# Optimization experiments

Hardware: AMD Instinct MI355X
Metric: run time of the kernel (lower is better)

Reference implementation:

```python
import jax, jax.numpy as jnp
import numpy as np

EPS_ROW = 1e-8
EPS_BN = 1e-5


def _row_norm(A):
    # A / clamp(rowsum, 1e-8)
    return A / jnp.clip(A.sum(axis=1, keepdims=True), EPS_ROW, None)


def _bn_eval(x, gamma, beta, mean, var):
    return (x - mean) * (gamma / jnp.sqrt(var + EPS_BN)) + beta


def setup_inputs() -> dict:
    key = jax.random.key(0)
    ks = jax.random.split(key, 12)
    n_src, n_tgt = 8192, 16384
    d_src, d_tgt_in, d_hid, d_out = 256, 128, 128, 64

    def xavier(k, fan_in, fan_out):
        lim = float(np.sqrt(6.0 / (fan_in + fan_out)))
        # stored as [in, out] so forward is x @ W + b
        return jax.random.uniform(k, (fan_in, fan_out), jnp.float32, -lim, lim)

    inp = {
        "H_source": jax.random.normal(ks[0], (n_src, d_src), jnp.float32),
        "H_target": jax.random.normal(ks[1], (n_tgt, d_tgt_in), jnp.float32),
        "A": jax.random.uniform(ks[2], (n_tgt, n_src), jnp.float32),
        "W0": xavier(ks[3], d_src, d_hid),
        "b0": jnp.zeros((d_hid,), jnp.float32),
        "Wb0": xavier(ks[4], d_hid, d_hid),
        "bb0": jnp.zeros((d_hid,), jnp.float32),
        "W1": xavier(ks[5], d_hid, d_hid),
        "b1": jnp.zeros((d_hid,), jnp.float32),
        # fwd BN layers (i=0 and i=2): stacked [2, d_hid]
        "bn_f_gamma": jax.random.uniform(ks[6], (2, d_hid), jnp.float32, 0.5, 1.5),
        "bn_f_beta": jax.random.normal(ks[7], (2, d_hid), jnp.float32) * 0.1,
        "bn_f_mean": jax.random.normal(ks[8], (2, d_hid), jnp.float32) * 0.1,
        "bn_f_var": jax.random.uniform(ks[9], (2, d_hid), jnp.float32, 0.5, 1.5),
        # bwd BN layer (i=1)
        "bn_b_gamma": jax.random.uniform(ks[10], (d_hid,), jnp.float32, 0.5, 1.5),
        "bn_b_beta": jnp.zeros((d_hid,), jnp.float32),
        "bn_b_mean": jnp.zeros((d_hid,), jnp.float32),
        "bn_b_var": jnp.ones((d_hid,), jnp.float32),
        "Wout": xavier(ks[11], d_hid, d_out),
        "bout": jnp.zeros((d_out,), jnp.float32),
    }
    return inp


def reference(H_source, H_target, A, W0, b0, Wb0, bb0, W1, b1,
              bn_f_gamma, bn_f_beta, bn_f_mean, bn_f_var,
              bn_b_gamma, bn_b_beta, bn_b_mean, bn_b_var,
              Wout, bout):
    # Inference mode: dropout = identity, BatchNorm uses running stats.
    A_n = _row_norm(A)          # [n_tgt, n_src]
    AT_n = _row_norm(A.T)       # [n_src, n_tgt]

    # layer 0 (fwd): target <- source
    h_tgt = (A_n @ H_source) @ W0 + b0
    h_tgt = jax.nn.relu(_bn_eval(h_tgt, bn_f_gamma[0], bn_f_beta[0], bn_f_mean[0], bn_f_var[0]))

    # layer 1 (bwd): source <- target
    h_src = (AT_n @ h_tgt) @ Wb0 + bb0
    h_src = jax.nn.relu(_bn_eval(h_src, bn_b_gamma, bn_b_beta, bn_b_mean, bn_b_var))

    # layer 2 (fwd): target <- source
    h_tgt = (A_n @ h_src) @ W1 + b1
    h_tgt = jax.nn.relu(_bn_eval(h_tgt, bn_f_gamma[1], bn_f_beta[1], bn_f_mean[1], bn_f_var[1]))

    return h_tgt @ Wout + bout  # [n_tgt, d_out]
```

## Files before the change

### kernel.cpp

```cpp
#include <hip/hip_runtime.h>
#include <hip/hip_bf16.h>
#include <stdint.h>

typedef unsigned short ushort_t;
typedef float   f32x4  __attribute__((ext_vector_type(4)));
typedef short   bf16x8 __attribute__((ext_vector_type(8)));

#define NSRC 8192
#define NTGT 16384

__device__ __forceinline__ ushort_t f2bf(float f){
  union { float f; uint32_t u; } v; v.f = f;
  uint32_t r = v.u + 0x7fffu + ((v.u >> 16) & 1u);
  return (ushort_t)(r >> 16);
}
__device__ __forceinline__ uint2 pack4(f32x4 v){
  uint2 r;
  r.x = (uint32_t)f2bf(v.x) | ((uint32_t)f2bf(v.y) << 16);
  r.y = (uint32_t)f2bf(v.z) | ((uint32_t)f2bf(v.w) << 16);
  return r;
}
__device__ __forceinline__ bf16x8 cvt8(f32x4 lo, f32x4 hi){
  union { uint4 u; bf16x8 h; } x;
  uint2 a = pack4(lo), b = pack4(hi);
  x.u = make_uint4(a.x, a.y, b.x, b.y);
  return x.h;
}
__device__ __forceinline__ uint4 asu4(bf16x8 v){ union { bf16x8 h; uint4 u; } x; x.h = v; return x.u; }
__device__ __forceinline__ float sum4(f32x4 v){ return v.x + v.y + v.z + v.w; }

typedef __attribute__((address_space(1))) const uint32_t* gas_t;
typedef __attribute__((address_space(3))) uint32_t* las_t;
__device__ __forceinline__ void dma16(const void* g, void* l){
  __builtin_amdgcn_global_load_lds((gas_t)g, (las_t)l, 16, 0, 0);
}
#define SCHED_FENCE() __builtin_amdgcn_sched_barrier(0)

__global__ __launch_bounds__(256) void k_wt(const float* __restrict__ S, ushort_t* __restrict__ D,
                                            int R, int C){
  __shared__ float tile[32][33];
  const int cb = blockIdx.x * 32, rb = blockIdx.y * 32;
  const int tx = threadIdx.x & 31, ty = threadIdx.x >> 5;
#pragma unroll
  for (int i = 0; i < 4; ++i)
    tile[ty + 8*i][tx] = S[(size_t)(rb + ty + 8*i) * C + cb + tx];
  __syncthreads();
#pragma unroll
  for (int i = 0; i < 4; ++i)
    D[(size_t)(cb + ty + 8*i) * R + rb + tx] = f2bf(tile[tx][ty + 8*i]);
}

__global__ __launch_bounds__(256) void k_packH(const float* __restrict__ S, ushort_t* __restrict__ D){
  int u = blockIdx.x * 4 + (threadIdx.x >> 6);
  int lane = threadIdx.x & 63;
  int nb = u >> 8, kb = u & 255;
  int fr = lane & 15, q = lane >> 4;
  ushort_t buf[8];
#pragma unroll
  for (int j = 0; j < 8; ++j)
    buf[j] = f2bf(S[(size_t)(kb * 32 + q * 8 + j) * 256 + nb * 16 + fr]);
  *(uint4*)&D[((size_t)nb * 256 + kb) * 512 + (size_t)lane * 8] = *(uint4*)buf;
}

__global__ void k_init_b2p_tail(ushort_t* __restrict__ B2p){
  int idx = blockIdx.x * 256 + threadIdx.x;
  int lane = idx & 63;
  int kb = idx >> 6;
  int fr = lane & 15;
  uint32_t v = (fr == 0) ? 0x3F803F80u : 0u;
  uint4 val = {v, v, v, v};
  *(uint4*)&B2p[((size_t)8 * 512 + kb) * 512 + (size_t)lane * 8] = val;
}

__global__ __launch_bounds__(512) void k_gemm1(const float* __restrict__ A,
    const ushort_t* __restrict__ B1p, float* __restrict__ P2, float* __restrict__ rowsumP,
    ushort_t* __restrict__ Abf){
  __shared__ ushort_t Bls[2][16 * 512];
  const int t = threadIdx.x;
  const int mb = blockIdx.x, kc = blockIdx.y;
  const size_t m0 = (size_t)mb * 128;
  const int k0 = kc * 2048;
  const int kb0 = k0 >> 5;

  const int w = t >> 6, lane = t & 63;
  const int wr = w >> 1, wc = w & 1;
  const int fr = lane & 15, q = lane >> 4;

  const float* pa0 = &A[(m0 + wr * 32 + fr) * (size_t)NSRC + k0 + q * 8];
  const float* pa1 = pa0 + (size_t)16 * NSRC;
  ushort_t* pw0 = &Abf[(m0 + wr * 32 + fr) * (size_t)NSRC + k0 + q * 8];
  ushort_t* pw1 = pw0 + (size_t)16 * NSRC;
  ushort_t* pw  = (wc == 0) ? pw0 : pw1;

  f32x4 acc[2][8];
  const f32x4 vz = {0.f, 0.f, 0.f, 0.f};
#pragma unroll
  for (int i = 0; i < 2; ++i)
#pragma unroll
    for (int j = 0; j < 8; ++j) acc[i][j] = vz;
  float rs0 = 0.f, rs1 = 0.f;

#pragma unroll
  for (int i = 0; i < 2; ++i){
    int f = w * 2 + i;
    dma16(&B1p[((size_t)f * 256 + kb0) * 512 + (size_t)lane * 8], &Bls[0][f * 512]);
  }
  SCHED_FENCE();
  f32x4 c0a = *(const f32x4*)pa0,        c0b = *(const f32x4*)(pa0 + 4);
  f32x4 c1a = *(const f32x4*)pa1,        c1b = *(const f32x4*)(pa1 + 4);
  f32x4 d0a = *(const f32x4*)(pa0 + 32), d0b = *(const f32x4*)(pa0 + 36);
  f32x4 d1a = *(const f32x4*)(pa1 + 32), d1b = *(const f32x4*)(pa1 + 36);
  asm volatile("s_waitcnt vmcnt(8)" ::: "memory");
  SCHED_FENCE();
  __builtin_amdgcn_s_barrier();

  for (int kt = 0; kt < 64; ++kt){
    const int cur = kt & 1;
    rs0 += sum4(c0a) + sum4(c0b);
    rs1 += sum4(c1a) + sum4(c1b);
    bf16x8 af0 = cvt8(c0a, c0b);
    bf16x8 af1 = cvt8(c1a, c1b);

    if (kt < 63){
#pragma unroll
      for (int i = 0; i < 2; ++i){
        int f = w * 2 + i;
        dma16(&B1p[((size_t)f * 256 + kb0 + kt + 1) * 512 + (size_t)lane * 8],
              &Bls[cur ^ 1][f * 512]);
      }
    }
    SCHED_FENCE();
    c0a = d0a; c0b = d0b; c1a = d1a; c1b = d1b;
    if (kt < 62){
      d0a = *(const f32x4*)(pa0 + (kt + 2) * 32); d0b = *(const f32x4*)(pa0 + (kt + 2) * 32 + 4);
      d1a = *(const f32x4*)(pa1 + (kt + 2) * 32); d1b = *(const f32x4*)(pa1 + (kt + 2) * 32 + 4);
    }
    *(uint4*)&pw[kt * 32] = asu4(wc == 0 ? af0 : af1);

#pragma unroll
    for (int fn = 0; fn < 8; ++fn){
      bf16x8 bfv = *(bf16x8*)&Bls[cur][(wc * 8 + fn) * 512 + lane * 8];
      acc[0][fn] = __builtin_amdgcn_mfma_f32_16x16x32_bf16(af0, bfv, acc[0][fn], 0, 0, 0);
      acc[1][fn] = __builtin_amdgcn_mfma_f32_16x16x32_bf16(af1, bfv, acc[1][fn], 0, 0, 0);
    }
    asm volatile("s_waitcnt vmcnt(5)" ::: "memory");
    SCHED_FENCE();
    __builtin_amdgcn_s_barrier();
  }

  float* Pd = P2 + (size_t)kc * NTGT * 256;
#pragma unroll
  for (int fm = 0; fm < 2; ++fm)
#pragma unroll
    for (int j = 0; j < 4; ++j){
      int row = wr * 32 + fm * 16 + q * 4 + j;
#pragma unroll
      for (int fn = 0; fn < 8; ++fn)
        Pd[(m0 + row) * 256 + wc * 128 + fn * 16 + fr] = acc[fm][fn][j];
    }

  rs0 += __shfl_xor(rs0, 16); rs0 += __shfl_xor(rs0, 32);
  rs1 += __shfl_xor(rs1, 16); rs1 += __shfl_xor(rs1, 32);
  if (wc == 0 && q == 0){
    rowsumP[(size_t)kc * NTGT + m0 + wr * 32 + fr]      = rs0;
    rowsumP[(size_t)kc * NTGT + m0 + wr * 32 + 16 + fr] = rs1;
  }
}

__global__ __launch_bounds__(512) void k_gemm2(const ushort_t* __restrict__ Abf,
    const ushort_t* __restrict__ B2p, float* __restrict__ G2p){
  __shared__ ushort_t Bls[2][9 * 512];
  const int t = threadIdx.x;
  const int sb = blockIdx.x, kc = blockIdx.y;
  const size_t s0 = (size_t)sb * 128;
  const int k0 = kc * 2048;
  const int kb0 = k0 >> 5;

  const int w = t >> 6, lane = t & 63;
  const int fr = lane & 15, q = lane >> 4;
  const size_t scol = s0 + w * 16 + fr;
  const ushort_t* pA = &Abf[(size_t)(k0 + q * 8) * NSRC + scol];

  f32x4 acc[9];
  const f32x4 vz = {0.f, 0.f, 0.f, 0.f};
#pragma unroll
  for (int j = 0; j < 9; ++j) acc[j] = vz;

#pragma unroll
  for (int i = 0; i < 2; ++i){
    int f = w + i * 8;
    if (f < 9)
      dma16(&B2p[((size_t)f * 512 + kb0) * 512 + (size_t)lane * 8], &Bls[0][f * 512]);
  }
  SCHED_FENCE();
  ushort_t aN[8], aX[8];
#pragma unroll
  for (int j = 0; j < 8; ++j) aN[j] = pA[(size_t)j * NSRC];
#pragma unroll
  for (int j = 0; j < 8; ++j) aX[j] = pA[(size_t)(32 + j) * NSRC];
  asm volatile("s_waitcnt vmcnt(16)" ::: "memory");
  SCHED_FENCE();
  __builtin_amdgcn_s_barrier();

  for (int kt = 0; kt < 64; ++kt){
    const int cur = kt & 1;
    bf16x8 af;
#pragma unroll
    for (int j = 0; j < 8; ++j) af[j] = (short)aN[j];

    if (kt < 63){
#pragma unroll
      for (int i = 0; i < 2; ++i){
        int f = w + i * 8;
        if (f < 9)
          dma16(&B2p[((size_t)f * 512 + kb0 + kt + 1) * 512 + (size_t)lane * 8],
                &Bls[cur ^ 1][f * 512]);
      }
    }
    SCHED_FENCE();
#pragma unroll
    for (int j = 0; j < 8; ++j) aN[j] = aX[j];
    if (kt < 62){
#pragma unroll
      for (int j = 0; j < 8; ++j)
        aX[j] = pA[((size_t)(kt + 2) * 32 + j) * NSRC];
    }

#pragma unroll
    for (int fn = 0; fn < 9; ++fn){
      bf16x8 bfv = *(bf16x8*)&Bls[cur][fn * 512 + lane * 8];
      acc[fn] = __builtin_amdgcn_mfma_f32_16x16x32_bf16(af, bfv, acc[fn], 0, 0, 0);
    }
    asm volatile("s_waitcnt vmcnt(8)" ::: "memory");
    SCHED_FENCE();
    __builtin_amdgcn_s_barrier();
  }

  float* Pd = G2p + (size_t)kc * NSRC * 144;
#pragma unroll
  for (int j = 0; j < 4; ++j){
    int row = w * 16 + q * 4 + j;
#pragma unroll
    for (int fn = 0; fn < 9; ++fn)
      Pd[(s0 + row) * 144 + fn * 16 + fr] = acc[fn][j];
  }
}

__global__ __launch_bounds__(512) void k_gemm3(const ushort_t* __restrict__ Abf,
    const ushort_t* __restrict__ B3p, float* __restrict__ G3p){
  __shared__ ushort_t Bls[2][8 * 512];
  const int t = threadIdx.x;
  const int mb = blockIdx.x, kc = blockIdx.y;
  const size_t m0 = (size_t)mb * 128;
  const int k0 = kc * 2048;
  const int kb0 = k0 >> 5;

  const int w = t >> 6, lane = t & 63;
  const int wr = w >> 1, wc = w & 1;
  const int fr = lane & 15, q = lane >> 4;

  const ushort_t* pa0 = &Abf[(m0 + wr * 32 + fr) * (size_t)NSRC + k0 + q * 8];
  const ushort_t* pa1 = pa0 + (size_t)16 * NSRC;

  f32x4 acc[2][4];
  const f32x4 vz = {0.f, 0.f, 0.f, 0.f};
#pragma unroll
  for (int i = 0; i < 2; ++i)
#pragma unroll
    for (int j = 0; j < 4; ++j) acc[i][j] = vz;

  dma16(&B3p[((size_t)w * 256 + kb0) * 512 + (size_t)lane * 8], &Bls[0][w * 512]);
  SCHED_FENCE();
  bf16x8 a0N = *(const bf16x8*)pa0;
  bf16x8 a1N = *(const bf16x8*)pa1;
  bf16x8 a0X = *(const bf16x8*)(pa0 + 32);
  bf16x8 a1X = *(const bf16x8*)(pa1 + 32);
  asm volatile("s_waitcnt vmcnt(4)" ::: "memory");
  SCHED_FENCE();
  __builtin_amdgcn_s_barrier();

  for (int kt = 0; kt < 64; ++kt){
    const int cur = kt & 1;
    bf16x8 u0 = a0N, u1 = a1N;

    if (kt < 63){
      dma16(&B3p[((size_t)w * 256 + kb0 + kt + 1) * 512 + (size_t)lane * 8],
            &Bls[cur ^ 1][w * 512]);
    }
    SCHED_FENCE();
    a0N = a0X; a1N = a1X;
    if (kt < 62){
      a0X = *(const bf16x8*)(pa0 + (kt + 2) * 32);
      a1X = *(const bf16x8*)(pa1 + (kt + 2) * 32);
    }

#pragma unroll
    for (int fn = 0; fn < 4; ++fn){
      bf16x8 bfv = *(bf16x8*)&Bls[cur][(wc * 4 + fn) * 512 + lane * 8];
      acc[0][fn] = __builtin_amdgcn_mfma_f32_16x16x32_bf16(u0, bfv, acc[0][fn], 0, 0, 0);
      acc[1][fn] = __builtin_amdgcn_mfma_f32_16x16x32_bf16(u1, bfv, acc[1][fn], 0, 0, 0);
    }
    asm volatile("s_waitcnt vmcnt(2)" ::: "memory");
    SCHED_FENCE();
    __builtin_amdgcn_s_barrier();
  }

  float* Pd = G3p + (size_t)kc * NTGT * 128;
#pragma unroll
  for (int fm = 0; fm < 2; ++fm)
#pragma unroll
    for (int j = 0; j < 4; ++j){
      int row = wr * 32 + fm * 16 + q * 4 + j;
#pragma unroll
      for (int fn = 0; fn < 4; ++fn)
        Pd[(m0 + row) * 128 + wc * 64 + fn * 16 + fr] = acc[fm][fn][j];
    }
}

__global__ __launch_bounds__(256) void k_s1(
    const float* __restrict__ P2, const float* __restrict__ rowsumP,
    const ushort_t* __restrict__ W0t, const float* __restrict__ b0,
    const float* __restrict__ g, const float* __restrict__ be,
    const float* __restrict__ mu, const float* __restrict__ va,
    ushort_t* __restrict__ B2p)
{
  __shared__ ushort_t Xs[64 * 72];
  __shared__ ushort_t Ws[128 * 72];
  __shared__ float    os[64 * 132];
  __shared__ float invs[64], scs[128], mbs[128];
  const int t = threadIdx.x;
  const size_t m0 = (size_t)blockIdx.x * 64;
  const size_t CH = (size_t)NTGT * 256;

  if (t < 64){
    float rsv = rowsumP[m0 + t] + rowsumP[(size_t)NTGT + m0 + t]
              + rowsumP[2 * (size_t)NTGT + m0 + t] + rowsumP[3 * (size_t)NTGT + m0 + t];
    invs[t] = 1.0f / fmaxf(rsv, 1e-8f);
  } else if (t < 192){
    int n = t - 64;
    float s = g[n] * rsqrtf(va[n] + 1e-5f);
    scs[n] = s;
    mbs[n] = (b0[n] - mu[n]) * s + be[n];
  }
  __syncthreads();

  const int w = t >> 6, lane = t & 63;
  const int wr = w >> 1, wc = w & 1;
  const int fr = lane & 15, q = lane >> 4;
  f32x4 acc[2][4];
  const f32x4 vz = {0.f, 0.f, 0.f, 0.f};
#pragma unroll
  for (int i = 0; i < 2; ++i)
#pragma unroll
    for (int j = 0; j < 4; ++j) acc[i][j] = vz;

  for (int kt = 0; kt < 4; ++kt){
    const int kk = kt * 64;
    __syncthreads();
#pragma unroll
    for (int r = 0; r < 4; ++r){
      int c = t + 256 * r;
      int row = c >> 4, col4 = (c & 15) * 4;
      const float* pa = &P2[(m0 + row) * 256 + kk + col4];
      f32x4 v0 = *(const f32x4*)pa;
      f32x4 v1 = *(const f32x4*)(pa + CH);
      f32x4 v2 = *(const f32x4*)(pa + 2 * CH);
      f32x4 v3 = *(const f32x4*)(pa + 3 * CH);
      f32x4 v = (v0 + v1 + v2 + v3) * invs[row];
      *(uint2*)&Xs[row * 72 + col4] = pack4(v);
    }
#pragma unroll
    for (int r = 0; r < 4; ++r){
      int c = t + 256 * r;
      int n = c >> 3, k8 = (c & 7) * 8;
      *(uint4*)&Ws[n * 72 + k8] = *(const uint4*)&W0t[(size_t)n * 256 + kk + k8];
    }
    __syncthreads();
#pragma unroll
    for (int ks = 0; ks < 2; ++ks){
      bf16x8 af[2], bfv[4];
      af[0] = *(const bf16x8*)&Xs[(wr * 32 + fr) * 72 + ks * 32 + q * 8];
      af[1] = *(const bf16x8*)&Xs[(wr * 32 + 16 + fr) * 72 + ks * 32 + q * 8];
#pragma unroll
      for (int fn = 0; fn < 4; ++fn)
        bfv[fn] = *(const bf16x8*)&Ws[(wc * 64 + fn * 16 + fr) * 72 + ks * 32 + q * 8];
#pragma unroll
      for (int fm = 0; fm < 2; ++fm)
#pragma unroll
        for (int fn = 0; fn < 4; ++fn)
          acc[fm][fn] = __builtin_amdgcn_mfma_f32_16x16x32_bf16(af[fm], bfv[fn], acc[fm][fn], 0, 0, 0);
    }
  }

#pragma unroll
  for (int fm = 0; fm < 2; ++fm)
#pragma unroll
    for (int fn = 0; fn < 4; ++fn){
      int n = wc * 64 + fn * 16 + fr;
      float s = scs[n], mb = mbs[n];
#pragma unroll
      for (int j = 0; j < 4; ++j){
        int row = wr * 32 + fm * 16 + q * 4 + j;
        os[row * 132 + n] = fmaxf(acc[fm][fn][j] * s + mb, 0.f);
      }
    }
  __syncthreads();
  {
    const int kb0 = (int)(m0 >> 5);
#pragma unroll
    for (int r = 0; r < 4; ++r){
      int s = t + 256 * r;
      int lane2 = s & 63;
      int kb2 = (s >> 6) & 1;
      int nb = s >> 7;
      int fr2 = lane2 & 15, q2 = lane2 >> 4;
      int n = nb * 16 + fr2;
      ushort_t buf[8];
#pragma unroll
      for (int j = 0; j < 8; ++j)
        buf[j] = f2bf(os[(kb2 * 32 + q2 * 8 + j) * 132 + n]);
      *(uint4*)&B2p[((size_t)nb * 512 + kb0 + kb2) * 512 + (size_t)lane2 * 8] = *(uint4*)buf;
    }
  }
}

__global__ __launch_bounds__(256) void k_s2(
    const float* __restrict__ G2p,
    const ushort_t* __restrict__ Wb0t, const float* __restrict__ bb0,
    const float* __restrict__ g, const float* __restrict__ be,
    const float* __restrict__ mu, const float* __restrict__ va,
    ushort_t* __restrict__ B3p)
{
  __shared__ ushort_t Xs[64 * 72];
  __shared__ ushort_t Ws[128 * 72];
  __shared__ float    os[64 * 132];
  __shared__ float invs[64], scs[128], mbs[128];
  const int t = threadIdx.x;
  const size_t m0 = (size_t)blockIdx.x * 64;
  const size_t CH = (size_t)NSRC * 144;

  if (t < 64){
    size_t row = m0 + t;
    float c = 0.f;
#pragma unroll
    for (int i = 0; i < 8; ++i) c += G2p[i * CH + row * 144 + 128];
    invs[t] = 1.0f / fmaxf(c, 1e-8f);
  } else if (t < 192){
    int n = t - 64;
    float s = g[n] * rsqrtf(va[n] + 1e-5f);
    scs[n] = s;
    mbs[n] = (bb0[n] - mu[n]) * s + be[n];
  }
  __syncthreads();

  const int w = t >> 6, lane = t & 63;
  const int wr = w >> 1, wc = w & 1;
  const int fr = lane & 15, q = lane >> 4;
  f32x4 acc[2][4];
  const f32x4 vz = {0.f, 0.f, 0.f, 0.f};
#pragma unroll
  for (int i = 0; i < 2; ++i)
#pragma unroll
    for (int j = 0; j < 4; ++j) acc[i][j] = vz;

  for (int kt = 0; kt < 2; ++kt){
    const int kk = kt * 64;
    __syncthreads();
#pragma unroll
    for (int r = 0; r < 4; ++r){
      int c = t + 256 * r;
      int row = c >> 4, col4 = (c & 15) * 4;
      const float* pa = &G2p[(m0 + row) * 144 + kk + col4];
      f32x4 v = {0.f, 0.f, 0.f, 0.f};
#pragma unroll
      for (int i = 0; i < 8; ++i) v += *(const f32x4*)(pa + i * CH);
      v *= invs[row];
      *(uint2*)&Xs[row * 72 + col4] = pack4(v);
    }
#pragma unroll
    for (int r = 0; r < 4; ++r){
      int c = t + 256 * r;
      int n = c >> 3, k8 = (c & 7) * 8;
      *(uint4*)&Ws[n * 72 + k8] = *(const uint4*)&Wb0t[(size_t)n * 128 + kk + k8];
    }
    __syncthreads();
#pragma unroll
    for (int ks = 0; ks < 2; ++ks){
      bf16x8 af[2], bfv[4];
      af[0] = *(const bf16x8*)&Xs[(wr * 32 + fr) * 72 + ks * 32 + q * 8];
      af[1] = *(const bf16x8*)&Xs[(wr * 32 + 16 + fr) * 72 + ks * 32 + q * 8];
#pragma unroll
      for (int fn = 0; fn < 4; ++fn)
        bfv[fn] = *(const bf16x8*)&Ws[(wc * 64 + fn * 16 + fr) * 72 + ks * 32 + q * 8];
#pragma unroll
      for (int fm = 0; fm < 2; ++fm)
#pragma unroll
        for (int fn = 0; fn < 4; ++fn)
          acc[fm][fn] = __builtin_amdgcn_mfma_f32_16x16x32_bf16(af[fm], bfv[fn], acc[fm][fn], 0, 0, 0);
    }
  }

#pragma unroll
  for (int fm = 0; fm < 2; ++fm)
#pragma unroll
    for (int fn = 0; fn < 4; ++fn){
      int n = wc * 64 + fn * 16 + fr;
      float s = scs[n], mb = mbs[n];
#pragma unroll
      for (int j = 0; j < 4; ++j){
        int row = wr * 32 + fm * 16 + q * 4 + j;
        os[row * 132 + n] = fmaxf(acc[fm][fn][j] * s + mb, 0.f);
      }
    }
  __syncthreads();
  {
    const int kb0 = (int)(m0 >> 5);
#pragma unroll
    for (int r = 0; r < 4; ++r){
      int s = t + 256 * r;
      int lane2 = s & 63;
      int kb2 = (s >> 6) & 1;
      int nb = s >> 7;
      int fr2 = lane2 & 15, q2 = lane2 >> 4;
      int n = nb * 16 + fr2;
      ushort_t buf[8];
#pragma unroll
      for (int j = 0; j < 8; ++j)
        buf[j] = f2bf(os[(kb2 * 32 + q2 * 8 + j) * 132 + n]);
      *(uint4*)&B3p[((size_t)nb * 256 + kb0 + kb2) * 512 + (size_t)lane2 * 8] = *(uint4*)buf;
    }
  }
}

__global__ __launch_bounds__(256) void k_s3(
    const float* __restrict__ G3p, const float* __restrict__ rowsumP,
    const ushort_t* __restrict__ W1t, const float* __restrict__ b1,
    const float* __restrict__ g, const float* __restrict__ be,
    const float* __restrict__ mu, const float* __restrict__ va,
    const ushort_t* __restrict__ Woutt, const float* __restrict__ bout,
    float* __restrict__ out)
{
  __shared__ ushort_t Xs[64 * 72];
  __shared__ ushort_t Ws[128 * 72];
  __shared__ ushort_t ys[64 * 136];
  __shared__ ushort_t Ws2[64 * 136];
  __shared__ float invs[64], scs[128], mbs[128];
  const int t = threadIdx.x;
  const size_t m0 = (size_t)blockIdx.x * 64;
  const size_t CH = (size_t)NTGT * 128;

  if (t < 64){
    float rsv = rowsumP[m0 + t] + rowsumP[(size_t)NTGT + m0 + t]
              + rowsumP[2 * (size_t)NTGT + m0 + t] + rowsumP[3 * (size_t)NTGT + m0 + t];
    invs[t] = 1.0f / fmaxf(rsv, 1e-8f);
  } else if (t < 192){
    int n = t - 64;
    float s = g[n] * rsqrtf(va[n] + 1e-5f);
    scs[n] = s;
    mbs[n] = (b1[n] - mu[n]) * s + be[n];
  }
#pragma unroll
  for (int r = 0; r < 4; ++r){
    int c = t + 256 * r;
    int n = c >> 4, k8 = (c & 15) * 8;
    *(uint4*)&Ws2[n * 136 + k8] = *(const uint4*)&Woutt[(size_t)n * 128 + k8];
  }
  __syncthreads();

  const int w = t >> 6, lane = t & 63;
  const int wr = w >> 1, wc = w & 1;
  const int fr = lane & 15, q = lane >> 4;
  f32x4 acc[2][4];
  const f32x4 vz = {0.f, 0.f, 0.f, 0.f};
#pragma unroll
  for (int i = 0; i < 2; ++i)
#pragma unroll
    for (int j = 0; j < 4; ++j) acc[i][j] = vz;

  for (int kt = 0; kt < 2; ++kt){
    const int kk = kt * 64;
    __syncthreads();
#pragma unroll
    for (int r = 0; r < 4; ++r){
      int c = t + 256 * r;
      int row = c >> 4, col4 = (c & 15) * 4;
      const float* pa = &G3p[(m0 + row) * 128 + kk + col4];
      f32x4 v0 = *(const f32x4*)pa;
      f32x4 v1 = *(const f32x4*)(pa + CH);
      f32x4 v2 = *(const f32x4*)(pa + 2 * CH);
      f32x4 v3 = *(const f32x4*)(pa + 3 * CH);
      f32x4 v = (v0 + v1 + v2 + v3) * invs[row];
      *(uint2*)&Xs[row * 72 + col4] = pack4(v);
    }
#pragma unroll
    for (int r = 0; r < 4; ++r){
      int c = t + 256 * r;
      int n = c >> 3, k8 = (c & 7) * 8;
      *(uint4*)&Ws[n * 72 + k8] = *(const uint4*)&W1t[(size_t)n * 128 + kk + k8];
    }
    __syncthreads();
#pragma unroll
    for (int ks = 0; ks < 2; ++ks){
      bf16x8 af[2], bfv[4];
      af[0] = *(const bf16x8*)&Xs[(wr * 32 + fr) * 72 + ks * 32 + q * 8];
      af[1] = *(const bf16x8*)&Xs[(wr * 32 + 16 + fr) * 72 + ks * 32 + q * 8];
#pragma unroll
      for (int fn = 0; fn < 4; ++fn)
        bfv[fn] = *(const bf16x8*)&Ws[(wc * 64 + fn * 16 + fr) * 72 + ks * 32 + q * 8];
#pragma unroll
      for (int fm = 0; fm < 2; ++fm)
#pragma unroll
        for (int fn = 0; fn < 4; ++fn)
          acc[fm][fn] = __builtin_amdgcn_mfma_f32_16x16x32_bf16(af[fm], bfv[fn], acc[fm][fn], 0, 0, 0);
    }
  }

#pragma unroll
  for (int fm = 0; fm < 2; ++fm)
#pragma unroll
    for (int fn = 0; fn < 4; ++fn){
      int n = wc * 64 + fn * 16 + fr;
      float s = scs[n], mb = mbs[n];
#pragma unroll
      for (int j = 0; j < 4; ++j){
        int row = wr * 32 + fm * 16 + q * 4 + j;
        ys[row * 136 + n] = f2bf(fmaxf(acc[fm][fn][j] * s + mb, 0.f));
      }
    }
  __syncthreads();

  f32x4 acc2[2][2];
#pragma unroll
  for (int i = 0; i < 2; ++i)
#pragma unroll
    for (int j = 0; j < 2; ++j) acc2[i][j] = vz;
#pragma unroll
  for (int ks = 0; ks < 4; ++ks){
    bf16x8 af[2], bfv[2];
    af[0] = *(const bf16x8*)&ys[(wr * 32 + fr) * 136 + ks * 32 + q * 8];
    af[1] = *(const bf16x8*)&ys[(wr * 32 + 16 + fr) * 136 + ks * 32 + q * 8];
#pragma unroll
    for (int fn = 0; fn < 2; ++fn)
      bfv[fn] = *(const bf16x8*)&Ws2[(wc * 32 + fn * 16 + fr) * 136 + ks * 32 + q * 8];
#pragma unroll
    for (int fm = 0; fm < 2; ++fm)
#pragma unroll
      for (int fn = 0; fn < 2; ++fn)
        acc2[fm][fn] = __builtin_amdgcn_mfma_f32_16x16x32_bf16(af[fm], bfv[fn], acc2[fm][fn], 0, 0, 0);
  }
#pragma unroll
  for (int fm = 0; fm < 2; ++fm)
#pragma unroll
    for (int fn = 0; fn < 2; ++fn){
      int n = wc * 32 + fn * 16 + fr;
      float bo = bout[n];
#pragma unroll
      for (int j = 0; j < 4; ++j){
        int row = wr * 32 + fm * 16 + q * 4 + j;
        out[(m0 + row) * 64 + n] = acc2[fm][fn][j] + bo;
      }
    }
}

extern "C" void kernel_launch(void* const* d_in, const int* in_sizes, int n_in,
                              void* d_out, int out_size, void* d_ws, size_t ws_size,
                              hipStream_t stream) {
  const float* Hs  = (const float*)d_in[0];
  const float* A   = (const float*)d_in[2];
  const float* W0  = (const float*)d_in[3];
  const float* b0  = (const float*)d_in[4];
  const float* Wb0 = (const float*)d_in[5];
  const float* bb0 = (const float*)d_in[6];
  const float* W1  = (const float*)d_in[7];
  const float* b1  = (const float*)d_in[8];
  const float* bnfg= (const float*)d_in[9];
  const float* bnfb= (const float*)d_in[10];
  const float* bnfm= (const float*)d_in[11];
  const float* bnfv= (const float*)d_in[12];
  const float* bnbg= (const float*)d_in[13];
  const float* bnbb= (const float*)d_in[14];
  const float* bnbm= (const float*)d_in[15];
  const float* bnbv= (const float*)d_in[16];
  const float* Wout= (const float*)d_in[17];
  const float* bout= (const float*)d_in[18];
  float* out = (float*)d_out;

  char* ws = (char*)d_ws;
  float*    R1    = (float*)ws;
  constexpr size_t OFF_ABF  = 67108864;
  constexpr size_t OFF_B1P  = OFF_ABF + 268435456;
  constexpr size_t OFF_B2P  = OFF_B1P + 4194304;
  constexpr size_t OFF_B3P  = OFF_B2P + 4718592;
  constexpr size_t OFF_RS   = OFF_B3P + 2097152;
  constexpr size_t OFF_W0T  = OFF_RS  + 262144;
  constexpr size_t OFF_WB0T = OFF_W0T + 65536;
  constexpr size_t OFF_W1T  = OFF_WB0T + 32768;
  constexpr size_t OFF_WOT  = OFF_W1T + 32768;
  ushort_t* Abf  = (ushort_t*)(ws + OFF_ABF);
  ushort_t* B1p  = (ushort_t*)(ws + OFF_B1P);
  ushort_t* B2p  = (ushort_t*)(ws + OFF_B2P);
  ushort_t* B3p  = (ushort_t*)(ws + OFF_B3P);
  float*    rsP  = (float*)   (ws + OFF_RS);
  ushort_t* W0t  = (ushort_t*)(ws + OFF_W0T);
  ushort_t* Wb0t = (ushort_t*)(ws + OFF_WB0T);
  ushort_t* W1t  = (ushort_t*)(ws + OFF_W1T);
  ushort_t* Wott = (ushort_t*)(ws + OFF_WOT);

  k_packH<<<1024, 256, 0, stream>>>(Hs, B1p);
  k_wt<<<dim3(128/32, 256/32),  256, 0, stream>>>(W0,  W0t, 256, 128);
  k_wt<<<dim3(128/32, 128/32),  256, 0, stream>>>(Wb0, Wb0t, 128, 128);
  k_wt<<<dim3(128/32, 128/32),  256, 0, stream>>>(W1,  W1t, 128, 128);
  k_wt<<<dim3(64/32, 128/32),   256, 0, stream>>>(Wout, Wott, 128, 64);
  k_init_b2p_tail<<<128, 256, 0, stream>>>(B2p);

  k_gemm1<<<dim3(128, 4), 512, 0, stream>>>(A, B1p, R1, rsP, Abf);
  k_s1<<<256, 256, 0, stream>>>(R1, rsP, W0t, b0, bnfg, bnfb, bnfm, bnfv, B2p);
  k_gemm2<<<dim3(64, 8), 512, 0, stream>>>(Abf, B2p, R1);
  k_s2<<<128, 256, 0, stream>>>(R1, Wb0t, bb0, bnbg, bnbb, bnbm, bnbv, B3p);
  k_gemm3<<<dim3(128, 4), 512, 0, stream>>>(Abf, B3p, R1);
  k_s3<<<256, 256, 0, stream>>>(R1, rsP, W1t, b1, bnfg + 128, bnfb + 128, bnfm + 128, bnfv + 128,
                                Wott, bout, out);
}
```

Measured before the change: 488.1 us.

## Double split-K factor, triple-buffer LDS B tiles, raise MFMA wave priority

Each of the three big GEMMs now splits K into twice as many chunks (8/16/8), so the grids have twice as many blocks to fill the GPU's compute units. The shared-memory B staging goes from double to triple buffering, prefetching two k-steps ahead with relaxed vmcnt waits, and MFMA sections are wrapped in s_setprio. The aim is more parallelism and more latency hiding on the memory-bound stream over A. In exchange, the split-K reduction stages read twice as many fp32 partials and the workspace grows.

```diff
diff --git a/kernel.cpp b/kernel.cpp
--- a/kernel.cpp
+++ b/kernel.cpp
@@ -8,6 +8,9 @@
 
 #define NSRC 8192
 #define NTGT 16384
+#define KS1 8
+#define KS2 16
+#define KS3 8
 
 __device__ __forceinline__ ushort_t f2bf(float f){
   union { float f; uint32_t u; } v; v.f = f;
@@ -75,11 +78,11 @@
 __global__ __launch_bounds__(512) void k_gemm1(const float* __restrict__ A,
     const ushort_t* __restrict__ B1p, float* __restrict__ P2, float* __restrict__ rowsumP,
     ushort_t* __restrict__ Abf){
-  __shared__ ushort_t Bls[2][16 * 512];
+  __shared__ ushort_t Bls[3][16 * 512];
   const int t = threadIdx.x;
   const int mb = blockIdx.x, kc = blockIdx.y;
   const size_t m0 = (size_t)mb * 128;
-  const int k0 = kc * 2048;
+  const int k0 = kc * 1024;
   const int kb0 = k0 >> 5;
 
   const int w = t >> 6, lane = t & 63;
@@ -105,47 +108,53 @@
     int f = w * 2 + i;
     dma16(&B1p[((size_t)f * 256 + kb0) * 512 + (size_t)lane * 8], &Bls[0][f * 512]);
   }
+#pragma unroll
+  for (int i = 0; i < 2; ++i){
+    int f = w * 2 + i;
+    dma16(&B1p[((size_t)f * 256 + kb0 + 1) * 512 + (size_t)lane * 8], &Bls[1][f * 512]);
+  }
   SCHED_FENCE();
   f32x4 c0a = *(const f32x4*)pa0,        c0b = *(const f32x4*)(pa0 + 4);
   f32x4 c1a = *(const f32x4*)pa1,        c1b = *(const f32x4*)(pa1 + 4);
   f32x4 d0a = *(const f32x4*)(pa0 + 32), d0b = *(const f32x4*)(pa0 + 36);
   f32x4 d1a = *(const f32x4*)(pa1 + 32), d1b = *(const f32x4*)(pa1 + 36);
-  asm volatile("s_waitcnt vmcnt(8)" ::: "memory");
+  asm volatile("s_waitcnt vmcnt(10)" ::: "memory");
   SCHED_FENCE();
   __builtin_amdgcn_s_barrier();
 
-  for (int kt = 0; kt < 64; ++kt){
-    const int cur = kt & 1;
+  int cur = 0;
+  for (int kt = 0; kt < 32; ++kt){
+    int nxt2 = cur + 2; if (nxt2 >= 3) nxt2 -= 3;
     rs0 += sum4(c0a) + sum4(c0b);
     rs1 += sum4(c1a) + sum4(c1b);
     bf16x8 af0 = cvt8(c0a, c0b);
     bf16x8 af1 = cvt8(c1a, c1b);
 
-    if (kt < 63){
-#pragma unroll
-      for (int i = 0; i < 2; ++i){
-        int f = w * 2 + i;
-        dma16(&B1p[((size_t)f * 256 + kb0 + kt + 1) * 512 + (size_t)lane * 8],
-              &Bls[cur ^ 1][f * 512]);
-      }
+    const int nt = (kt + 2 <= 31) ? (kt + 2) : 31;
+#pragma unroll
+    for (int i = 0; i < 2; ++i){
+      int f = w * 2 + i;
+      dma16(&B1p[((size_t)f * 256 + kb0 + nt) * 512 + (size_t)lane * 8],
+            &Bls[nxt2][f * 512]);
     }
     SCHED_FENCE();
     c0a = d0a; c0b = d0b; c1a = d1a; c1b = d1b;
-    if (kt < 62){
-      d0a = *(const f32x4*)(pa0 + (kt + 2) * 32); d0b = *(const f32x4*)(pa0 + (kt + 2) * 32 + 4);
-      d1a = *(const f32x4*)(pa1 + (kt + 2) * 32); d1b = *(const f32x4*)(pa1 + (kt + 2) * 32 + 4);
-    }
+    d0a = *(const f32x4*)(pa0 + nt * 32); d0b = *(const f32x4*)(pa0 + nt * 32 + 4);
+    d1a = *(const f32x4*)(pa1 + nt * 32); d1b = *(const f32x4*)(pa1 + nt * 32 + 4);
     *(uint4*)&pw[kt * 32] = asu4(wc == 0 ? af0 : af1);
 
+    __builtin_amdgcn_s_setprio(1);
 #pragma unroll
     for (int fn = 0; fn < 8; ++fn){
       bf16x8 bfv = *(bf16x8*)&Bls[cur][(wc * 8 + fn) * 512 + lane * 8];
       acc[0][fn] = __builtin_amdgcn_mfma_f32_16x16x32_bf16(af0, bfv, acc[0][fn], 0, 0, 0);
       acc[1][fn] = __builtin_amdgcn_mfma_f32_16x16x32_bf16(af1, bfv, acc[1][fn], 0, 0, 0);
     }
-    asm volatile("s_waitcnt vmcnt(5)" ::: "memory");
+    __builtin_amdgcn_s_setprio(0);
+    asm volatile("s_waitcnt vmcnt(12)" ::: "memory");
     SCHED_FENCE();
     __builtin_amdgcn_s_barrier();
+    cur = (cur == 2) ? 0 : cur + 1;
   }
 
   float* Pd = P2 + (size_t)kc * NTGT * 256;
@@ -169,11 +178,11 @@
 
 __global__ __launch_bounds__(512) void k_gemm2(const ushort_t* __restrict__ Abf,
     const ushort_t* __restrict__ B2p, float* __restrict__ G2p){
-  __shared__ ushort_t Bls[2][9 * 512];
+  __shared__ ushort_t Bls[3][9 * 512];
   const int t = threadIdx.x;
   const int sb = blockIdx.x, kc = blockIdx.y;
   const size_t s0 = (size_t)sb * 128;
-  const int k0 = kc * 2048;
+  const int k0 = kc * 1024;
   const int kb0 = k0 >> 5;
 
   const int w = t >> 6, lane = t & 63;
@@ -186,12 +195,12 @@
 #pragma unroll
   for (int j = 0; j < 9; ++j) acc[j] = vz;
 
-#pragma unroll
-  for (int i = 0; i < 2; ++i){
-    int f = w + i * 8;
-    if (f < 9)
-      dma16(&B2p[((size_t)f * 512 + kb0) * 512 + (size_t)lane * 8], &Bls[0][f * 512]);
-  }
+  dma16(&B2p[((size_t)w * 512 + kb0) * 512 + (size_t)lane * 8], &Bls[0][w * 512]);
+  if (w == 0)
+    dma16(&B2p[((size_t)8 * 512 + kb0) * 512 + (size_t)lane * 8], &Bls[0][8 * 512]);
+  dma16(&B2p[((size_t)w * 512 + kb0 + 1) * 512 + (size_t)lane * 8], &Bls[1][w * 512]);
+  if (w == 0)
+    dma16(&B2p[((size_t)8 * 512 + kb0 + 1) * 512 + (size_t)lane * 8], &Bls[1][8 * 512]);
   SCHED_FENCE();
   ushort_t aN[8], aX[8];
 #pragma unroll
@@ -202,38 +211,35 @@
   SCHED_FENCE();
   __builtin_amdgcn_s_barrier();
 
-  for (int kt = 0; kt < 64; ++kt){
-    const int cur = kt & 1;
+  int cur = 0;
+  for (int kt = 0; kt < 32; ++kt){
+    int nxt2 = cur + 2; if (nxt2 >= 3) nxt2 -= 3;
     bf16x8 af;
 #pragma unroll
     for (int j = 0; j < 8; ++j) af[j] = (short)aN[j];
 
-    if (kt < 63){
-#pragma unroll
-      for (int i = 0; i < 2; ++i){
-        int f = w + i * 8;
-        if (f < 9)
-          dma16(&B2p[((size_t)f * 512 + kb0 + kt + 1) * 512 + (size_t)lane * 8],
-                &Bls[cur ^ 1][f * 512]);
-      }
-    }
+    const int nt = (kt + 2 <= 31) ? (kt + 2) : 31;
+    dma16(&B2p[((size_t)w * 512 + kb0 + nt) * 512 + (size_t)lane * 8], &Bls[nxt2][w * 512]);
+    if (w == 0)
+      dma16(&B2p[((size_t)8 * 512 + kb0 + nt) * 512 + (size_t)lane * 8], &Bls[nxt2][8 * 512]);
     SCHED_FENCE();
 #pragma unroll
     for (int j = 0; j < 8; ++j) aN[j] = aX[j];
-    if (kt < 62){
-#pragma unroll
-      for (int j = 0; j < 8; ++j)
-        aX[j] = pA[((size_t)(kt + 2) * 32 + j) * NSRC];
-    }
-
+#pragma unroll
+    for (int j = 0; j < 8; ++j)
+      aX[j] = pA[((size_t)nt * 32 + j) * NSRC];
+
+    __builtin_amdgcn_s_setprio(1);
 #pragma unroll
     for (int fn = 0; fn < 9; ++fn){
       bf16x8 bfv = *(bf16x8*)&Bls[cur][fn * 512 + lane * 8];
       acc[fn] = __builtin_amdgcn_mfma_f32_16x16x32_bf16(af, bfv, acc[fn], 0, 0, 0);
     }
-    asm volatile("s_waitcnt vmcnt(8)" ::: "memory");
+    __builtin_amdgcn_s_setprio(0);
+    asm volatile("s_waitcnt vmcnt(16)" ::: "memory");
     SCHED_FENCE();
     __builtin_amdgcn_s_barrier();
+    cur = (cur == 2) ? 0 : cur + 1;
   }
 
   float* Pd = G2p + (size_t)kc * NSRC * 144;
@@ -248,11 +254,11 @@
 
 __global__ __launch_bounds__(512) void k_gemm3(const ushort_t* __restrict__ Abf,
     const ushort_t* __restrict__ B3p, float* __restrict__ G3p){
-  __shared__ ushort_t Bls[2][8 * 512];
+  __shared__ ushort_t Bls[3][8 * 512];
   const int t = threadIdx.x;
   const int mb = blockIdx.x, kc = blockIdx.y;
   const size_t m0 = (size_t)mb * 128;
-  const int k0 = kc * 2048;
+  const int k0 = kc * 1024;
   const int kb0 = k0 >> 5;
 
   const int w = t >> 6, lane = t & 63;
@@ -270,39 +276,40 @@
     for (int j = 0; j < 4; ++j) acc[i][j] = vz;
 
   dma16(&B3p[((size_t)w * 256 + kb0) * 512 + (size_t)lane * 8], &Bls[0][w * 512]);
+  dma16(&B3p[((size_t)w * 256 + kb0 + 1) * 512 + (size_t)lane * 8], &Bls[1][w * 512]);
   SCHED_FENCE();
   bf16x8 a0N = *(const bf16x8*)pa0;
   bf16x8 a1N = *(const bf16x8*)pa1;
   bf16x8 a0X = *(const bf16x8*)(pa0 + 32);
   bf16x8 a1X = *(const bf16x8*)(pa1 + 32);
-  asm volatile("s_waitcnt vmcnt(4)" ::: "memory");
+  asm volatile("s_waitcnt vmcnt(5)" ::: "memory");
   SCHED_FENCE();
   __builtin_amdgcn_s_barrier();
 
-  for (int kt = 0; kt < 64; ++kt){
-    const int cur = kt & 1;
+  int cur = 0;
+  for (int kt = 0; kt < 32; ++kt){
+    int nxt2 = cur + 2; if (nxt2 >= 3) nxt2 -= 3;
     bf16x8 u0 = a0N, u1 = a1N;
 
-    if (kt < 63){
-      dma16(&B3p[((size_t)w * 256 + kb0 + kt + 1) * 512 + (size_t)lane * 8],
-            &Bls[cur ^ 1][w * 512]);
-    }
+    const int nt = (kt + 2 <= 31) ? (kt + 2) : 31;
+    dma16(&B3p[((size_t)w * 256 + kb0 + nt) * 512 + (size_t)lane * 8], &Bls[nxt2][w * 512]);
     SCHED_FENCE();
     a0N = a0X; a1N = a1X;
-    if (kt < 62){
-      a0X = *(const bf16x8*)(pa0 + (kt + 2) * 32);
-      a1X = *(const bf16x8*)(pa1 + (kt + 2) * 32);
-    }
-
+    a0X = *(const bf16x8*)(pa0 + nt * 32);
+    a1X = *(const bf16x8*)(pa1 + nt * 32);
+
+    __builtin_amdgcn_s_setprio(1);
 #pragma unroll
     for (int fn = 0; fn < 4; ++fn){
       bf16x8 bfv = *(bf16x8*)&Bls[cur][(wc * 4 + fn) * 512 + lane * 8];
       acc[0][fn] = __builtin_amdgcn_mfma_f32_16x16x32_bf16(u0, bfv, acc[0][fn], 0, 0, 0);
       acc[1][fn] = __builtin_amdgcn_mfma_f32_16x16x32_bf16(u1, bfv, acc[1][fn], 0, 0, 0);
     }
-    asm volatile("s_waitcnt vmcnt(2)" ::: "memory");
+    __builtin_amdgcn_s_setprio(0);
+    asm volatile("s_waitcnt vmcnt(5)" ::: "memory");
     SCHED_FENCE();
     __builtin_amdgcn_s_barrier();
+    cur = (cur == 2) ? 0 : cur + 1;
   }
 
   float* Pd = G3p + (size_t)kc * NTGT * 128;
@@ -333,8 +340,9 @@
   const size_t CH = (size_t)NTGT * 256;
 
   if (t < 64){
-    float rsv = rowsumP[m0 + t] + rowsumP[(size_t)NTGT + m0 + t]
-              + rowsumP[2 * (size_t)NTGT + m0 + t] + rowsumP[3 * (size_t)NTGT + m0 + t];
+    float rsv = 0.f;
+#pragma unroll
+    for (int i = 0; i < KS1; ++i) rsv += rowsumP[(size_t)i * NTGT + m0 + t];
     invs[t] = 1.0f / fmaxf(rsv, 1e-8f);
   } else if (t < 192){
     int n = t - 64;
@@ -362,11 +370,10 @@
       int c = t + 256 * r;
       int row = c >> 4, col4 = (c & 15) * 4;
       const float* pa = &P2[(m0 + row) * 256 + kk + col4];
-      f32x4 v0 = *(const f32x4*)pa;
-      f32x4 v1 = *(const f32x4*)(pa + CH);
-      f32x4 v2 = *(const f32x4*)(pa + 2 * CH);
-      f32x4 v3 = *(const f32x4*)(pa + 3 * CH);
-      f32x4 v = (v0 + v1 + v2 + v3) * invs[row];
+      f32x4 v = {0.f, 0.f, 0.f, 0.f};
+#pragma unroll
+      for (int i = 0; i < KS1; ++i) v += *(const f32x4*)(pa + (size_t)i * CH);
+      v *= invs[row];
       *(uint2*)&Xs[row * 72 + col4] = pack4(v);
     }
 #pragma unroll
@@ -443,7 +450,7 @@
     size_t row = m0 + t;
     float c = 0.f;
 #pragma unroll
-    for (int i = 0; i < 8; ++i) c += G2p[i * CH + row * 144 + 128];
+    for (int i = 0; i < KS2; ++i) c += G2p[(size_t)i * CH + row * 144 + 128];
     invs[t] = 1.0f / fmaxf(c, 1e-8f);
   } else if (t < 192){
     int n = t - 64;
@@ -473,7 +480,7 @@
       const float* pa = &G2p[(m0 + row) * 144 + kk + col4];
       f32x4 v = {0.f, 0.f, 0.f, 0.f};
 #pragma unroll
-      for (int i = 0; i < 8; ++i) v += *(const f32x4*)(pa + i * CH);
+      for (int i = 0; i < KS2; ++i) v += *(const f32x4*)(pa + (size_t)i * CH);
       v *= invs[row];
       *(uint2*)&Xs[row * 72 + col4] = pack4(v);
     }
@@ -550,8 +557,9 @@
   const size_t CH = (size_t)NTGT * 128;
 
   if (t < 64){
-    float rsv = rowsumP[m0 + t] + rowsumP[(size_t)NTGT + m0 + t]
-              + rowsumP[2 * (size_t)NTGT + m0 + t] + rowsumP[3 * (size_t)NTGT + m0 + t];
+    float rsv = 0.f;
+#pragma unroll
+    for (int i = 0; i < KS1; ++i) rsv += rowsumP[(size_t)i * NTGT + m0 + t];
     invs[t] = 1.0f / fmaxf(rsv, 1e-8f);
   } else if (t < 192){
     int n = t - 64;
@@ -585,11 +593,10 @@
       int c = t + 256 * r;
       int row = c >> 4, col4 = (c & 15) * 4;
       const float* pa = &G3p[(m0 + row) * 128 + kk + col4];
-      f32x4 v0 = *(const f32x4*)pa;
-      f32x4 v1 = *(const f32x4*)(pa + CH);
-      f32x4 v2 = *(const f32x4*)(pa + 2 * CH);
-      f32x4 v3 = *(const f32x4*)(pa + 3 * CH);
-      f32x4 v = (v0 + v1 + v2 + v3) * invs[row];
+      f32x4 v = {0.f, 0.f, 0.f, 0.f};
+#pragma unroll
+      for (int i = 0; i < KS3; ++i) v += *(const f32x4*)(pa + (size_t)i * CH);
+      v *= invs[row];
       *(uint2*)&Xs[row * 72 + col4] = pack4(v);
     }
 #pragma unroll
@@ -687,12 +694,12 @@
 
   char* ws = (char*)d_ws;
   float*    R1    = (float*)ws;
-  constexpr size_t OFF_ABF  = 67108864;
+  constexpr size_t OFF_ABF  = 134217728;
   constexpr size_t OFF_B1P  = OFF_ABF + 268435456;
   constexpr size_t OFF_B2P  = OFF_B1P + 4194304;
   constexpr size_t OFF_B3P  = OFF_B2P + 4718592;
   constexpr size_t OFF_RS   = OFF_B3P + 2097152;
-  constexpr size_t OFF_W0T  = OFF_RS  + 262144;
+  constexpr size_t OFF_W0T  = OFF_RS  + 524288;
   constexpr size_t OFF_WB0T = OFF_W0T + 65536;
   constexpr size_t OFF_W1T  = OFF_WB0T + 32768;
   constexpr size_t OFF_WOT  = OFF_W1T + 32768;
@@ -713,11 +720,11 @@
   k_wt<<<dim3(64/32, 128/32),   256, 0, stream>>>(Wout, Wott, 128, 64);
   k_init_b2p_tail<<<128, 256, 0, stream>>>(B2p);
 
-  k_gemm1<<<dim3(128, 4), 512, 0, stream>>>(A, B1p, R1, rsP, Abf);
+  k_gemm1<<<dim3(128, KS1), 512, 0, stream>>>(A, B1p, R1, rsP, Abf);
   k_s1<<<256, 256, 0, stream>>>(R1, rsP, W0t, b0, bnfg, bnfb, bnfm, bnfv, B2p);
-  k_gemm2<<<dim3(64, 8), 512, 0, stream>>>(Abf, B2p, R1);
+  k_gemm2<<<dim3(64, KS2), 512, 0, stream>>>(Abf, B2p, R1);
   k_s2<<<128, 256, 0, stream>>>(R1, Wb0t, bb0, bnbg, bnbb, bnbm, bnbv, B3p);
-  k_gemm3<<<dim3(128, 4), 512, 0, stream>>>(Abf, B3p, R1);
+  k_gemm3<<<dim3(128, KS3), 512, 0, stream>>>(Abf, B3p, R1);
   k_s3<<<256, 256, 0, stream>>>(R1, rsP, W1t, b1, bnfg + 128, bnfb + 128, bnfm + 128, bnfv + 128,
                                 Wott, bout, out);
 }
```

Result: slower. 682.6 us (+39.9%).
